# Optimization experiments

Measured on AMD Instinct MI355X. Metric: run time of the kernel, lower is better.

The kernel has to match this reference:

```python
import jax, jax.numpy as jnp
import numpy as np

N_AGENTS, OBS_DIM, HID, ACT_DIM = 8192, 64, 128, 16


def setup_inputs() -> dict:
    key = jax.random.key(0)
    k = jax.random.split(key, 8)
    obs_agents = jax.random.normal(k[0], (N_AGENTS, OBS_DIM), dtype=jnp.float32)
    # binary adjacency, {0,1}, int32 (index/mask semantics, non-differentiable)
    adj = jax.random.randint(k[1], (N_AGENTS, N_AGENTS), 0, 2, dtype=jnp.int32)
    def lin(kk, fan_in, fan_out):
        lim = 1.0 / np.sqrt(fan_in)
        kw, kb = jax.random.split(kk)
        W = jax.random.uniform(kw, (fan_in, fan_out), jnp.float32, -lim, lim)
        b = jax.random.uniform(kb, (fan_out,), jnp.float32, -lim, lim)
        return W, b
    W1, b1 = lin(k[2], OBS_DIM, HID)          # encoder
    W2, b2 = lin(k[3], 2 * HID, HID)          # actor layer 1
    W3, b3 = lin(k[4], HID, ACT_DIM)          # actor layer 2
    return {"obs_agents": obs_agents, "adj": adj,
            "W1": W1, "b1": b1, "W2": W2, "b2": b2, "W3": W3, "b3": b3}


def reference(obs_agents, adj, W1, b1, W2, b2, W3, b3):
    # per-agent encode: h = tanh(obs @ W1 + b1)  -> [N, HID]
    h = jnp.tanh(obs_agents @ W1 + b1)
    # neighbor mean message: mean of h[j] over j with adj[i,j]!=0, zeros if no neighbors
    a = adj.astype(h.dtype)                      # [N, N] binary
    deg = jnp.sum(a, axis=1, keepdims=True)      # [N, 1]
    msg = (a @ h) / jnp.maximum(deg, 1.0)        # zero rows stay zero
    # actor MLP on concat([h, msg])
    combined = jnp.concatenate([h, msg], axis=-1)            # [N, 2*HID]
    hid = jnp.tanh(combined @ W2 + b2)                        # [N, HID]
    logits = hid @ W3 + b3                                    # [N, ACT_DIM]
    return logits
```

## Files before the change

### kernel.cpp

```cpp
#include <hip/hip_runtime.h>
#include <stdint.h>
#include <math.h>

#define NAG 8192
#define NB  144
#define BM  64
#define NSPLIT 8

typedef __attribute__((ext_vector_type(8))) short short8;
typedef __attribute__((ext_vector_type(4))) float floatx4;

__device__ __forceinline__ float bf2f(unsigned short u) {
    union { uint32_t i; float f; } v; v.i = ((uint32_t)u) << 16; return v.f;
}
__device__ __forceinline__ unsigned short f2bf(float f) {
    union { float f; uint32_t i; } v; v.f = f;
    uint32_t x = v.i;
    return (unsigned short)((x + 0x7FFFu + ((x >> 16) & 1u)) >> 16);
}
__device__ __forceinline__ unsigned short f2h(float f) {
    union { _Float16 h; unsigned short u; } v; v.h = (_Float16)f; return v.u;
}
__device__ __forceinline__ float h2f(unsigned short u) {
    union { _Float16 h; unsigned short u; } v; v.u = u; return (float)v.h;
}
__device__ __forceinline__ void gload_lds16(const void* g, void* lds) {
    __builtin_amdgcn_global_load_lds(
        (const __attribute__((address_space(1))) uint32_t*)g,
        (__attribute__((address_space(3))) uint32_t*)lds, 16, 0, 0);
}

__global__ __launch_bounds__(64) void k0_init(
    int* __restrict__ flag, const unsigned short* __restrict__ W1raw)
{
    int big = 0;
    #pragma unroll
    for (int j = 0; j < 8; ++j) {
        float v = bf2f(W1raw[threadIdx.x * 8 + j]);
        if (!(fabsf(v) <= 1e6f)) big = 1;
    }
    unsigned long long m = __ballot(big);
    if (threadIdx.x == 0) *flag = (m != 0ull) ? 1 : 0;
}

__global__ __launch_bounds__(256) void k1_encode(
    const void* __restrict__ obs,
    const void* __restrict__ W1,
    const void* __restrict__ b1,
    const int* __restrict__ flag,
    float* __restrict__ h_f32,
    unsigned short* __restrict__ hT)
{
    __shared__ float obs_lds[32][68];
    __shared__ unsigned short ht_lds[128][33];
    const int t = threadIdx.x;
    const int abase = blockIdx.x * 32;
    const bool isf = (*flag != 0);

    {
        int a = t >> 3, c0 = (t & 7) * 8;
        if (isf) {
            const float* p = (const float*)obs;
            #pragma unroll
            for (int j = 0; j < 8; ++j)
                obs_lds[a][c0 + j] = p[(size_t)(abase + a) * 64 + c0 + j];
        } else {
            const unsigned short* p = (const unsigned short*)obs;
            #pragma unroll
            for (int j = 0; j < 8; ++j)
                obs_lds[a][c0 + j] = bf2f(p[(size_t)(abase + a) * 64 + c0 + j]);
        }
    }
    __syncthreads();

    const int o = t & 127;
    const int half = t >> 7;
    float acc[16];
    if (isf) {
        const float* Wp = (const float*)W1;
        float bias = ((const float*)b1)[o];
        #pragma unroll
        for (int i = 0; i < 16; ++i) acc[i] = bias;
        for (int k0 = 0; k0 < 64; k0 += 8) {
            float w[8];
            #pragma unroll
            for (int j = 0; j < 8; ++j) w[j] = Wp[(k0 + j) * 128 + o];
            #pragma unroll
            for (int j = 0; j < 8; ++j)
                #pragma unroll
                for (int i = 0; i < 16; ++i)
                    acc[i] = fmaf(obs_lds[half * 16 + i][k0 + j], w[j], acc[i]);
        }
    } else {
        const unsigned short* Wp = (const unsigned short*)W1;
        float bias = bf2f(((const unsigned short*)b1)[o]);
        #pragma unroll
        for (int i = 0; i < 16; ++i) acc[i] = bias;
        for (int k0 = 0; k0 < 64; k0 += 8) {
            float w[8];
            #pragma unroll
            for (int j = 0; j < 8; ++j) w[j] = bf2f(Wp[(k0 + j) * 128 + o]);
            #pragma unroll
            for (int j = 0; j < 8; ++j)
                #pragma unroll
                for (int i = 0; i < 16; ++i)
                    acc[i] = fmaf(obs_lds[half * 16 + i][k0 + j], w[j], acc[i]);
        }
    }
    #pragma unroll
    for (int i = 0; i < 16; ++i) {
        float th = tanhf(acc[i]);
        int a = half * 16 + i;
        h_f32[(size_t)(abase + a) * 128 + o] = th;
        ht_lds[o][a] = f2bf(th);
    }
    __syncthreads();

    for (int p = 0; p < 18; ++p) {
        int n = p * 8 + (t >> 5);
        int a = t & 31;
        unsigned short v;
        if (n < 128)       v = ht_lds[n][a];
        else if (n == 128) v = 0x3F80;
        else               v = 0;
        hT[(size_t)n * NAG + abase + a] = v;
    }
}

__global__ __launch_bounds__(256, 4) void k2_msggemm(
    const int* __restrict__ adj,
    const unsigned short* __restrict__ hT,
    unsigned short* __restrict__ Cp16)
{
    __shared__ __align__(16) int Alds[64 * 64];
    __shared__ __align__(16) unsigned short Blds[144 * 64];
    const int t = threadIdx.x;
    const int mtile = blockIdx.x & 127;
    const int ks = blockIdx.x >> 7;
    const int row0 = mtile * BM;
    const int kbeg = ks * 1024;

    const int wave = t >> 6, lane = t & 63;
    const int fm = lane & 15, quad = lane >> 4;

    floatx4 acc[9];
    #pragma unroll
    for (int i = 0; i < 9; ++i) acc[i] = (floatx4)0.f;

    const int ra0 = 16 * wave + (lane >> 4);
    const int* a0 = adj + (size_t)(row0 + ra0 +  0) * NAG + kbeg + (((lane & 15) ^ ((ra0 +  0) & 15)) << 2);
    const int* a1 = adj + (size_t)(row0 + ra0 +  4) * NAG + kbeg + (((lane & 15) ^ ((ra0 +  4) & 15)) << 2);
    const int* a2 = adj + (size_t)(row0 + ra0 +  8) * NAG + kbeg + (((lane & 15) ^ ((ra0 +  8) & 15)) << 2);
    const int* a3 = adj + (size_t)(row0 + ra0 + 12) * NAG + kbeg + (((lane & 15) ^ ((ra0 + 12) & 15)) << 2);
    const int rb0 = 32 * wave + (lane >> 3);
    const int bco = (((lane & 7) ^ ((lane >> 3) & 7)) << 3);
    const unsigned short* b0 = hT + (size_t)(rb0 +  0) * NAG + kbeg + bco;
    const unsigned short* b1 = hT + (size_t)(rb0 +  8) * NAG + kbeg + bco;
    const unsigned short* b2 = hT + (size_t)(rb0 + 16) * NAG + kbeg + bco;
    const unsigned short* b3 = hT + (size_t)(rb0 + 24) * NAG + kbeg + bco;
    int* Ad0 = &Alds[(wave * 4 + 0) * 256];
    int* Ad1 = &Alds[(wave * 4 + 1) * 256];
    int* Ad2 = &Alds[(wave * 4 + 2) * 256];
    int* Ad3 = &Alds[(wave * 4 + 3) * 256];
    unsigned short* Bd0 = &Blds[(wave * 4 + 0) * 512];
    unsigned short* Bd1 = &Blds[(wave * 4 + 1) * 512];
    unsigned short* Bd2 = &Blds[(wave * 4 + 2) * 512];
    unsigned short* Bd3 = &Blds[(wave * 4 + 3) * 512];

    {
        int rr = 128 + (t >> 4);
        int off = (t & 15) * 4;
        uint32_t vv = (rr == 128) ? 0x3F803F80u : 0u;
        *reinterpret_cast<uint2*>(&Blds[rr * 64 + off]) = make_uint2(vv, vv);
    }

    for (int it = 0; it < 16; ++it) {
        const int ko = it * 64;
        __syncthreads();
        gload_lds16(a0 + ko, Ad0);
        gload_lds16(a1 + ko, Ad1);
        gload_lds16(a2 + ko, Ad2);
        gload_lds16(a3 + ko, Ad3);
        gload_lds16(b0 + ko, Bd0);
        gload_lds16(b1 + ko, Bd1);
        gload_lds16(b2 + ko, Bd2);
        gload_lds16(b3 + ko, Bd3);
        __syncthreads();
        #pragma unroll
        for (int kk = 0; kk < 64; kk += 32) {
            const int arow = (wave * 16 + fm) * 64;
            const int c0 = (kk >> 2) + 2 * quad;
            int4 v0 = *reinterpret_cast<const int4*>(&Alds[arow + (((c0 + 0) ^ fm) << 2)]);
            int4 v1 = *reinterpret_cast<const int4*>(&Alds[arow + (((c0 + 1) ^ fm) << 2)]);
            union { uint32_t u[4]; short8 s; } af;
            af.u[0] = ((uint32_t)v0.x | ((uint32_t)v0.y << 16)) * 0x3F80u;
            af.u[1] = ((uint32_t)v0.z | ((uint32_t)v0.w << 16)) * 0x3F80u;
            af.u[2] = ((uint32_t)v1.x | ((uint32_t)v1.y << 16)) * 0x3F80u;
            af.u[3] = ((uint32_t)v1.z | ((uint32_t)v1.w << 16)) * 0x3F80u;
            const int bc = (kk >> 3) + quad;
            #pragma unroll
            for (int j = 0; j < 9; ++j) {
                int rb = j * 16 + fm;
                short8 bf = *reinterpret_cast<const short8*>(&Blds[rb * 64 + ((bc ^ (fm & 7)) << 3)]);
                acc[j] = __builtin_amdgcn_mfma_f32_16x16x32_bf16(af.s, bf, acc[j], 0, 0, 0);
            }
        }
    }

    unsigned short* out = Cp16 + (size_t)ks * (NAG * NB);
    #pragma unroll
    for (int j = 0; j < 9; ++j) {
        int col = j * 16 + fm;
        #pragma unroll
        for (int r = 0; r < 4; ++r) {
            int row = row0 + wave * 16 + quad * 4 + r;
            out[(size_t)row * NB + col] = f2h(acc[j][r]);
        }
    }
}

__global__ __launch_bounds__(256) void k3_actor(
    const float* __restrict__ h_f32,
    const unsigned short* __restrict__ Cp16,
    const void* __restrict__ W2,
    const void* __restrict__ b2,
    const void* __restrict__ W3,
    const void* __restrict__ b3,
    const int* __restrict__ flag,
    void* __restrict__ out)
{
    __shared__ float4 comb4[16][66];
    __shared__ float hid[16][132];
    __shared__ float inv_lds[16];
    const int t = threadIdx.x;
    const int abase = blockIdx.x * 16;
    const bool isf = (*flag != 0);
    const size_t PS = (size_t)NAG * NB;

    if (t < 16) {
        float deg = 0.f;
        #pragma unroll
        for (int s = 0; s < NSPLIT; ++s)
            deg += h2f(Cp16[s * PS + (size_t)(abase + t) * NB + 128]);
        inv_lds[t] = 1.0f / fmaxf(deg, 1.0f);
    }
    __syncthreads();

    #pragma unroll
    for (int jj = 0; jj < 4; ++jj) {
        int idx = jj * 256 + t;
        int a = idx >> 6, q = idx & 63;
        float4 v;
        if (q < 32) {
            v = *reinterpret_cast<const float4*>(h_f32 + (size_t)(abase + a) * 128 + q * 4);
        } else {
            int f = (q - 32) * 4;
            float s0 = 0.f, s1 = 0.f, s2 = 0.f, s3 = 0.f;
            #pragma unroll
            for (int s = 0; s < NSPLIT; ++s) {
                ushort4 p = *reinterpret_cast<const ushort4*>(Cp16 + s * PS + (size_t)(abase + a) * NB + f);
                s0 += h2f(p.x); s1 += h2f(p.y); s2 += h2f(p.z); s3 += h2f(p.w);
            }
            float sc = inv_lds[a];
            v = make_float4(s0 * sc, s1 * sc, s2 * sc, s3 * sc);
        }
        comb4[a][q] = v;
    }
    __syncthreads();

    const int o = t & 127, half = t >> 7;
    float acc[8];
    if (isf) {
        const float* Wp = (const float*)W2;
        float bias = ((const float*)b2)[o];
        #pragma unroll
        for (int i = 0; i < 8; ++i) acc[i] = bias;
        for (int cq = 0; cq < 64; ++cq) {
            float w0 = Wp[(cq * 4 + 0) * 128 + o];
            float w1 = Wp[(cq * 4 + 1) * 128 + o];
            float w2 = Wp[(cq * 4 + 2) * 128 + o];
            float w3 = Wp[(cq * 4 + 3) * 128 + o];
            #pragma unroll
            for (int i = 0; i < 8; ++i) {
                float4 v = comb4[half * 8 + i][cq];
                acc[i] = fmaf(v.x, w0, acc[i]);
                acc[i] = fmaf(v.y, w1, acc[i]);
                acc[i] = fmaf(v.z, w2, acc[i]);
                acc[i] = fmaf(v.w, w3, acc[i]);
            }
        }
    } else {
        const unsigned short* Wp = (const unsigned short*)W2;
        float bias = bf2f(((const unsigned short*)b2)[o]);
        #pragma unroll
        for (int i = 0; i < 8; ++i) acc[i] = bias;
        for (int cq = 0; cq < 64; ++cq) {
            float w0 = bf2f(Wp[(cq * 4 + 0) * 128 + o]);
            float w1 = bf2f(Wp[(cq * 4 + 1) * 128 + o]);
            float w2 = bf2f(Wp[(cq * 4 + 2) * 128 + o]);
            float w3 = bf2f(Wp[(cq * 4 + 3) * 128 + o]);
            #pragma unroll
            for (int i = 0; i < 8; ++i) {
                float4 v = comb4[half * 8 + i][cq];
                acc[i] = fmaf(v.x, w0, acc[i]);
                acc[i] = fmaf(v.y, w1, acc[i]);
                acc[i] = fmaf(v.z, w2, acc[i]);
                acc[i] = fmaf(v.w, w3, acc[i]);
            }
        }
    }
    #pragma unroll
    for (int i = 0; i < 8; ++i)
        hid[half * 8 + i][o] = tanhf(acc[i]);
    __syncthreads();

    const int q = t & 15, ar = t >> 4;
    float l;
    if (isf) {
        const float* Wp = (const float*)W3;
        l = ((const float*)b3)[q];
        #pragma unroll 4
        for (int oo = 0; oo < 128; ++oo)
            l = fmaf(hid[ar][oo], Wp[oo * 16 + q], l);
    } else {
        const unsigned short* Wp = (const unsigned short*)W3;
        l = bf2f(((const unsigned short*)b3)[q]);
        #pragma unroll 4
        for (int oo = 0; oo < 128; ++oo)
            l = fmaf(hid[ar][oo], bf2f(Wp[oo * 16 + q]), l);
    }
    size_t i0 = (size_t)(abase + ar) * 16 + q;
    if (isf) ((float*)out)[i0] = l;
    else     ((unsigned short*)out)[i0] = f2bf(l);
}

extern "C" void kernel_launch(void* const* d_in, const int* in_sizes, int n_in,
                              void* d_out, int out_size, void* d_ws, size_t ws_size,
                              hipStream_t stream) {
    const void* obs = d_in[0];
    const int*  adj = (const int*)d_in[1];
    const void* W1  = d_in[2];
    const void* b1  = d_in[3];
    const void* W2  = d_in[4];
    const void* b2  = d_in[5];
    const void* W3  = d_in[6];
    const void* b3  = d_in[7];

    char* ws = (char*)d_ws;
    unsigned short* hT   = (unsigned short*)(ws);
    float*          h_f32= (float*)(ws + 2359296);
    unsigned short* Cp16 = (unsigned short*)(ws + 6553600);
    int*            flag = (int*)(ws + 25427968);

    hipLaunchKernelGGL(k0_init, dim3(1), dim3(64), 0, stream, flag, (const unsigned short*)W1);
    hipLaunchKernelGGL(k1_encode, dim3(256), dim3(256), 0, stream, obs, W1, b1, flag, h_f32, hT);
    hipLaunchKernelGGL(k2_msggemm, dim3(1024), dim3(256), 0, stream, adj, hT, Cp16);
    hipLaunchKernelGGL(k3_actor, dim3(512), dim3(256), 0, stream, h_f32, Cp16, W2, b2, W3, b3, flag, d_out);
}
```

Baseline: 467.0 us.

## Double-buffer LDS tiles in message GEMM to overlap loads with MFMA

```diff
diff --git a/kernel.cpp b/kernel.cpp
--- a/kernel.cpp
+++ b/kernel.cpp
@@ -5,6 +5,7 @@
 #define NAG 8192
 #define NB  144
 #define BM  64
+#define BK  32
 #define NSPLIT 8
 
 typedef __attribute__((ext_vector_type(8))) short short8;
@@ -132,8 +133,10 @@
     const unsigned short* __restrict__ hT,
     unsigned short* __restrict__ Cp16)
 {
-    __shared__ __align__(16) int Alds[64 * 64];
-    __shared__ __align__(16) unsigned short Blds[144 * 64];
+    __shared__ __align__(16) int Alds0[64 * BK];
+    __shared__ __align__(16) int Alds1[64 * BK];
+    __shared__ __align__(16) unsigned short Blds0[144 * BK];
+    __shared__ __align__(16) unsigned short Blds1[144 * BK];
     const int t = threadIdx.x;
     const int mtile = blockIdx.x & 127;
     const int ks = blockIdx.x >> 7;
@@ -147,64 +150,59 @@
     #pragma unroll
     for (int i = 0; i < 9; ++i) acc[i] = (floatx4)0.f;
 
-    const int ra0 = 16 * wave + (lane >> 4);
-    const int* a0 = adj + (size_t)(row0 + ra0 +  0) * NAG + kbeg + (((lane & 15) ^ ((ra0 +  0) & 15)) << 2);
-    const int* a1 = adj + (size_t)(row0 + ra0 +  4) * NAG + kbeg + (((lane & 15) ^ ((ra0 +  4) & 15)) << 2);
-    const int* a2 = adj + (size_t)(row0 + ra0 +  8) * NAG + kbeg + (((lane & 15) ^ ((ra0 +  8) & 15)) << 2);
-    const int* a3 = adj + (size_t)(row0 + ra0 + 12) * NAG + kbeg + (((lane & 15) ^ ((ra0 + 12) & 15)) << 2);
-    const int rb0 = 32 * wave + (lane >> 3);
-    const int bco = (((lane & 7) ^ ((lane >> 3) & 7)) << 3);
-    const unsigned short* b0 = hT + (size_t)(rb0 +  0) * NAG + kbeg + bco;
-    const unsigned short* b1 = hT + (size_t)(rb0 +  8) * NAG + kbeg + bco;
-    const unsigned short* b2 = hT + (size_t)(rb0 + 16) * NAG + kbeg + bco;
-    const unsigned short* b3 = hT + (size_t)(rb0 + 24) * NAG + kbeg + bco;
-    int* Ad0 = &Alds[(wave * 4 + 0) * 256];
-    int* Ad1 = &Alds[(wave * 4 + 1) * 256];
-    int* Ad2 = &Alds[(wave * 4 + 2) * 256];
-    int* Ad3 = &Alds[(wave * 4 + 3) * 256];
-    unsigned short* Bd0 = &Blds[(wave * 4 + 0) * 512];
-    unsigned short* Bd1 = &Blds[(wave * 4 + 1) * 512];
-    unsigned short* Bd2 = &Blds[(wave * 4 + 2) * 512];
-    unsigned short* Bd3 = &Blds[(wave * 4 + 3) * 512];
+    const int rowA = wave * 8 + (lane >> 3);
+    const int cA = (lane & 7) ^ (rowA & 7);
+    const int* aS0 = adj + (size_t)(row0 + rowA) * NAG + kbeg + cA * 4;
+    const int* aS1 = adj + (size_t)(row0 + rowA + 32) * NAG + kbeg + cA * 4;
+    const int rowB = wave * 16 + (lane >> 2);
+    const int cB = (lane & 3) ^ ((rowB >> 1) & 3);
+    const unsigned short* bS0 = hT + (size_t)rowB * NAG + kbeg + cB * 8;
+    const unsigned short* bS1 = hT + (size_t)(rowB + 64) * NAG + kbeg + cB * 8;
+    int* Ad00 = Alds0 + wave * 256;  int* Ad01 = Alds0 + 1024 + wave * 256;
+    int* Ad10 = Alds1 + wave * 256;  int* Ad11 = Alds1 + 1024 + wave * 256;
+    unsigned short* Bd00 = Blds0 + wave * 512;  unsigned short* Bd01 = Blds0 + 2048 + wave * 512;
+    unsigned short* Bd10 = Blds1 + wave * 512;  unsigned short* Bd11 = Blds1 + 2048 + wave * 512;
 
     {
         int rr = 128 + (t >> 4);
-        int off = (t & 15) * 4;
+        int off = (t & 15) * 2;
         uint32_t vv = (rr == 128) ? 0x3F803F80u : 0u;
-        *reinterpret_cast<uint2*>(&Blds[rr * 64 + off]) = make_uint2(vv, vv);
-    }
-
-    for (int it = 0; it < 16; ++it) {
-        const int ko = it * 64;
+        *reinterpret_cast<uint32_t*>(&Blds0[rr * BK + off]) = vv;
+        *reinterpret_cast<uint32_t*>(&Blds1[rr * BK + off]) = vv;
+    }
+
+#define DMA(T, Ad0_, Ad1_, Bd0_, Bd1_) do { \
+        gload_lds16(aS0 + (T) * BK, (Ad0_)); \
+        gload_lds16(aS1 + (T) * BK, (Ad1_)); \
+        gload_lds16(bS0 + (T) * BK, (Bd0_)); \
+        gload_lds16(bS1 + (T) * BK, (Bd1_)); \
+    } while (0)
+#define COMPUTE(Ab, Bb) do { \
+        const int arow = (wave * 16 + fm) * BK; \
+        int4 v0 = *reinterpret_cast<const int4*>(&(Ab)[arow + (((quad * 2 + 0) ^ (fm & 7)) << 2)]); \
+        int4 v1 = *reinterpret_cast<const int4*>(&(Ab)[arow + (((quad * 2 + 1) ^ (fm & 7)) << 2)]); \
+        union { uint32_t u[4]; short8 s; } af; \
+        af.u[0] = ((uint32_t)v0.x | ((uint32_t)v0.y << 16)) * 0x3F80u; \
+        af.u[1] = ((uint32_t)v0.z | ((uint32_t)v0.w << 16)) * 0x3F80u; \
+        af.u[2] = ((uint32_t)v1.x | ((uint32_t)v1.y << 16)) * 0x3F80u; \
+        af.u[3] = ((uint32_t)v1.z | ((uint32_t)v1.w << 16)) * 0x3F80u; \
+        const int bphys = (quad ^ ((fm >> 1) & 3)) << 3; \
+        _Pragma("unroll") \
+        for (int j = 0; j < 9; ++j) { \
+            short8 bf = *reinterpret_cast<const short8*>(&(Bb)[(j * 16 + fm) * BK + bphys]); \
+            acc[j] = __builtin_amdgcn_mfma_f32_16x16x32_bf16(af.s, bf, acc[j], 0, 0, 0); \
+        } \
+    } while (0)
+
+    DMA(0, Ad00, Ad01, Bd00, Bd01);
+
+    for (int it = 0; it < 32; it += 2) {
         __syncthreads();
-        gload_lds16(a0 + ko, Ad0);
-        gload_lds16(a1 + ko, Ad1);
-        gload_lds16(a2 + ko, Ad2);
-        gload_lds16(a3 + ko, Ad3);
-        gload_lds16(b0 + ko, Bd0);
-        gload_lds16(b1 + ko, Bd1);
-        gload_lds16(b2 + ko, Bd2);
-        gload_lds16(b3 + ko, Bd3);
+        DMA(it + 1, Ad10, Ad11, Bd10, Bd11);
+        COMPUTE(Alds0, Blds0);
         __syncthreads();
-        #pragma unroll
-        for (int kk = 0; kk < 64; kk += 32) {
-            const int arow = (wave * 16 + fm) * 64;
-            const int c0 = (kk >> 2) + 2 * quad;
-            int4 v0 = *reinterpret_cast<const int4*>(&Alds[arow + (((c0 + 0) ^ fm) << 2)]);
-            int4 v1 = *reinterpret_cast<const int4*>(&Alds[arow + (((c0 + 1) ^ fm) << 2)]);
-            union { uint32_t u[4]; short8 s; } af;
-            af.u[0] = ((uint32_t)v0.x | ((uint32_t)v0.y << 16)) * 0x3F80u;
-            af.u[1] = ((uint32_t)v0.z | ((uint32_t)v0.w << 16)) * 0x3F80u;
-            af.u[2] = ((uint32_t)v1.x | ((uint32_t)v1.y << 16)) * 0x3F80u;
-            af.u[3] = ((uint32_t)v1.z | ((uint32_t)v1.w << 16)) * 0x3F80u;
-            const int bc = (kk >> 3) + quad;
-            #pragma unroll
-            for (int j = 0; j < 9; ++j) {
-                int rb = j * 16 + fm;
-                short8 bf = *reinterpret_cast<const short8*>(&Blds[rb * 64 + ((bc ^ (fm & 7)) << 3)]);
-                acc[j] = __builtin_amdgcn_mfma_f32_16x16x32_bf16(af.s, bf, acc[j], 0, 0, 0);
-            }
-        }
+        if (it + 2 < 32) DMA(it + 2, Ad00, Ad01, Bd00, Bd01);
+        COMPUTE(Alds1, Blds1);
     }
 
     unsigned short* out = Cp16 + (size_t)ks * (NAG * NB);
@@ -217,6 +215,8 @@
             out[(size_t)row * NB + col] = f2h(acc[j][r]);
         }
     }
+#undef DMA
+#undef COMPUTE
 }
 
 __global__ __launch_bounds__(256) void k3_actor(
```

Result: no change. 469.7 us (+0.6%).

## Stream adjacency directly into registers and stage hT slice once per block

Applied to the files above, without the earlier changes.

```diff
diff --git a/kernel.cpp b/kernel.cpp
--- a/kernel.cpp
+++ b/kernel.cpp
@@ -4,8 +4,9 @@
 
 #define NAG 8192
 #define NB  144
-#define BM  64
-#define NSPLIT 8
+#define BM  128
+#define NSPLIT 32
+#define LDB 264
 
 typedef __attribute__((ext_vector_type(8))) short short8;
 typedef __attribute__((ext_vector_type(4))) float floatx4;
@@ -23,11 +24,6 @@
 }
 __device__ __forceinline__ float h2f(unsigned short u) {
     union { _Float16 h; unsigned short u; } v; v.u = u; return (float)v.h;
-}
-__device__ __forceinline__ void gload_lds16(const void* g, void* lds) {
-    __builtin_amdgcn_global_load_lds(
-        (const __attribute__((address_space(1))) uint32_t*)g,
-        (__attribute__((address_space(3))) uint32_t*)lds, 16, 0, 0);
 }
 
 __global__ __launch_bounds__(64) void k0_init(
@@ -127,83 +123,48 @@
     }
 }
 
-__global__ __launch_bounds__(256, 4) void k2_msggemm(
+__global__ __launch_bounds__(512, 4) void k2_msggemm(
     const int* __restrict__ adj,
     const unsigned short* __restrict__ hT,
     unsigned short* __restrict__ Cp16)
 {
-    __shared__ __align__(16) int Alds[64 * 64];
-    __shared__ __align__(16) unsigned short Blds[144 * 64];
+    __shared__ __align__(16) unsigned short Blds[144 * LDB];
     const int t = threadIdx.x;
-    const int mtile = blockIdx.x & 127;
-    const int ks = blockIdx.x >> 7;
+    const int mtile = blockIdx.x & 63;
+    const int ks = blockIdx.x >> 6;
     const int row0 = mtile * BM;
-    const int kbeg = ks * 1024;
+    const int kbeg = ks * 256;
 
     const int wave = t >> 6, lane = t & 63;
     const int fm = lane & 15, quad = lane >> 4;
 
+    #pragma unroll
+    for (int i = 0; i < 9; ++i) {
+        int idx = i * 512 + t;
+        int row = idx >> 5, ch = idx & 31;
+        uint4 v = *reinterpret_cast<const uint4*>(hT + (size_t)row * NAG + kbeg + ch * 8);
+        *reinterpret_cast<uint4*>(&Blds[row * LDB + ch * 8]) = v;
+    }
+    __syncthreads();
+
     floatx4 acc[9];
     #pragma unroll
     for (int i = 0; i < 9; ++i) acc[i] = (floatx4)0.f;
 
-    const int ra0 = 16 * wave + (lane >> 4);
-    const int* a0 = adj + (size_t)(row0 + ra0 +  0) * NAG + kbeg + (((lane & 15) ^ ((ra0 +  0) & 15)) << 2);
-    const int* a1 = adj + (size_t)(row0 + ra0 +  4) * NAG + kbeg + (((lane & 15) ^ ((ra0 +  4) & 15)) << 2);
-    const int* a2 = adj + (size_t)(row0 + ra0 +  8) * NAG + kbeg + (((lane & 15) ^ ((ra0 +  8) & 15)) << 2);
-    const int* a3 = adj + (size_t)(row0 + ra0 + 12) * NAG + kbeg + (((lane & 15) ^ ((ra0 + 12) & 15)) << 2);
-    const int rb0 = 32 * wave + (lane >> 3);
-    const int bco = (((lane & 7) ^ ((lane >> 3) & 7)) << 3);
-    const unsigned short* b0 = hT + (size_t)(rb0 +  0) * NAG + kbeg + bco;
-    const unsigned short* b1 = hT + (size_t)(rb0 +  8) * NAG + kbeg + bco;
-    const unsigned short* b2 = hT + (size_t)(rb0 + 16) * NAG + kbeg + bco;
-    const unsigned short* b3 = hT + (size_t)(rb0 + 24) * NAG + kbeg + bco;
-    int* Ad0 = &Alds[(wave * 4 + 0) * 256];
-    int* Ad1 = &Alds[(wave * 4 + 1) * 256];
-    int* Ad2 = &Alds[(wave * 4 + 2) * 256];
-    int* Ad3 = &Alds[(wave * 4 + 3) * 256];
-    unsigned short* Bd0 = &Blds[(wave * 4 + 0) * 512];
-    unsigned short* Bd1 = &Blds[(wave * 4 + 1) * 512];
-    unsigned short* Bd2 = &Blds[(wave * 4 + 2) * 512];
-    unsigned short* Bd3 = &Blds[(wave * 4 + 3) * 512];
-
-    {
-        int rr = 128 + (t >> 4);
-        int off = (t & 15) * 4;
-        uint32_t vv = (rr == 128) ? 0x3F803F80u : 0u;
-        *reinterpret_cast<uint2*>(&Blds[rr * 64 + off]) = make_uint2(vv, vv);
-    }
-
-    for (int it = 0; it < 16; ++it) {
-        const int ko = it * 64;
-        __syncthreads();
-        gload_lds16(a0 + ko, Ad0);
-        gload_lds16(a1 + ko, Ad1);
-        gload_lds16(a2 + ko, Ad2);
-        gload_lds16(a3 + ko, Ad3);
-        gload_lds16(b0 + ko, Bd0);
-        gload_lds16(b1 + ko, Bd1);
-        gload_lds16(b2 + ko, Bd2);
-        gload_lds16(b3 + ko, Bd3);
-        __syncthreads();
-        #pragma unroll
-        for (int kk = 0; kk < 64; kk += 32) {
-            const int arow = (wave * 16 + fm) * 64;
-            const int c0 = (kk >> 2) + 2 * quad;
-            int4 v0 = *reinterpret_cast<const int4*>(&Alds[arow + (((c0 + 0) ^ fm) << 2)]);
-            int4 v1 = *reinterpret_cast<const int4*>(&Alds[arow + (((c0 + 1) ^ fm) << 2)]);
-            union { uint32_t u[4]; short8 s; } af;
-            af.u[0] = ((uint32_t)v0.x | ((uint32_t)v0.y << 16)) * 0x3F80u;
-            af.u[1] = ((uint32_t)v0.z | ((uint32_t)v0.w << 16)) * 0x3F80u;
-            af.u[2] = ((uint32_t)v1.x | ((uint32_t)v1.y << 16)) * 0x3F80u;
-            af.u[3] = ((uint32_t)v1.z | ((uint32_t)v1.w << 16)) * 0x3F80u;
-            const int bc = (kk >> 3) + quad;
-            #pragma unroll
-            for (int j = 0; j < 9; ++j) {
-                int rb = j * 16 + fm;
-                short8 bf = *reinterpret_cast<const short8*>(&Blds[rb * 64 + ((bc ^ (fm & 7)) << 3)]);
-                acc[j] = __builtin_amdgcn_mfma_f32_16x16x32_bf16(af.s, bf, acc[j], 0, 0, 0);
-            }
+    const int* aP = adj + (size_t)(row0 + wave * 16 + fm) * NAG + kbeg + quad * 8;
+
+    for (int w = 0; w < 8; ++w) {
+        int4 v0 = *reinterpret_cast<const int4*>(aP + w * 32);
+        int4 v1 = *reinterpret_cast<const int4*>(aP + w * 32 + 4);
+        union { uint32_t u[4]; short8 s; } af;
+        af.u[0] = ((uint32_t)v0.x | ((uint32_t)v0.y << 16)) * 0x3F80u;
+        af.u[1] = ((uint32_t)v0.z | ((uint32_t)v0.w << 16)) * 0x3F80u;
+        af.u[2] = ((uint32_t)v1.x | ((uint32_t)v1.y << 16)) * 0x3F80u;
+        af.u[3] = ((uint32_t)v1.z | ((uint32_t)v1.w << 16)) * 0x3F80u;
+        #pragma unroll
+        for (int j = 0; j < 9; ++j) {
+            short8 bf = *reinterpret_cast<const short8*>(&Blds[(j * 16 + fm) * LDB + w * 32 + quad * 8]);
+            acc[j] = __builtin_amdgcn_mfma_f32_16x16x32_bf16(af.s, bf, acc[j], 0, 0, 0);
         }
     }
 
@@ -350,10 +311,10 @@
     unsigned short* hT   = (unsigned short*)(ws);
     float*          h_f32= (float*)(ws + 2359296);
     unsigned short* Cp16 = (unsigned short*)(ws + 6553600);
-    int*            flag = (int*)(ws + 25427968);
+    int*            flag = (int*)(ws + 82051072);
 
     hipLaunchKernelGGL(k0_init, dim3(1), dim3(64), 0, stream, flag, (const unsigned short*)W1);
     hipLaunchKernelGGL(k1_encode, dim3(256), dim3(256), 0, stream, obs, W1, b1, flag, h_f32, hT);
-    hipLaunchKernelGGL(k2_msggemm, dim3(1024), dim3(256), 0, stream, adj, hT, Cp16);
+    hipLaunchKernelGGL(k2_msggemm, dim3(2048), dim3(512), 0, stream, adj, hT, Cp16);
     hipLaunchKernelGGL(k3_actor, dim3(512), dim3(256), 0, stream, h_f32, Cp16, W2, b2, W3, b3, flag, d_out);
 }
```

New measurement: 457.8 us. 1.02x faster.
